# Optimization experiments

Hardware: AMD Instinct MI355X
Metric: run time of the kernel (lower is better)

The kernel has to match this reference:

```python
import jax, jax.numpy as jnp
import numpy as np

N = 50000
IN_CH = 64
HID_CH = 32
NEG_SLOPE = 0.2  # PyG GATConv default for attention LeakyReLU


def _glorot(key, shape):
    fan = shape[0] + shape[-1] if len(shape) > 1 else shape[0]
    s = jnp.sqrt(6.0 / fan)
    return jax.random.uniform(key, shape, jnp.float32, -s, s)


def setup_inputs() -> dict:
    key = jax.random.key(0)
    ks = jax.random.split(key, 20)
    x = jax.random.normal(ks[0], (N, IN_CH), jnp.float32)
    edge_index = jax.random.randint(ks[1], (2, 800000), 0, N, jnp.int64)
    dims = [(IN_CH, IN_CH), (IN_CH, HID_CH), (HID_CH, IN_CH), (IN_CH, IN_CH)]
    inp = {"x": x, "edge_index": edge_index}
    for i, (di, do) in enumerate(dims, 1):
        inp[f"w{i}"] = _glorot(ks[4 * i - 2], (di, do))
        inp[f"as{i}"] = _glorot(ks[4 * i - 1], (do,))
        inp[f"ad{i}"] = _glorot(ks[4 * i], (do,))
        inp[f"b{i}"] = jnp.zeros((do,), jnp.float32)
    return inp


def _gat_layer(x, src, dst, W, a_src, a_dst, b):
    # x: [N, di] -> h: [N, do]
    h = x @ W
    # per-edge attention logits (source + destination contributions)
    e = jax.nn.leaky_relu(h[src] @ a_src + h[dst] @ a_dst, NEG_SLOPE)  # [E]
    # numerically stable segment softmax over incoming edges per dst node
    m = jax.ops.segment_max(e, dst, num_segments=N)
    ex = jnp.exp(e - m[dst])
    denom = jax.ops.segment_sum(ex, dst, num_segments=N)
    alpha = ex / (denom[dst] + 1e-16)  # [E]
    out = jax.ops.segment_sum(alpha[:, None] * h[src], dst, num_segments=N)
    return out + b


def reference(x, edge_index, w1, as1, ad1, b1, w2, as2, ad2, b2,
              w3, as3, ad3, b3, w4, as4, ad4, b4):
    # PyG GATConv adds self-loops by default
    ar = jnp.arange(N, dtype=edge_index.dtype)
    src = jnp.concatenate([edge_index[0], ar])
    dst = jnp.concatenate([edge_index[1], ar])

    h1 = jax.nn.relu(_gat_layer(x, src, dst, w1, as1, ad1, b1))
    h = _gat_layer(h1, src, dst, w2, as2, ad2, b2)
    h3 = jax.nn.relu(h)
    h4 = jax.nn.relu(_gat_layer(h3, src, dst, w3, as3, ad3, b3))
    out = _gat_layer(h4, src, dst, w4, as4, ad4, b4)
    return (out, h)
```

## Files before the change

### kernel.cpp

```cpp
#include <hip/hip_runtime.h>
#include <hip/hip_fp16.h>
#include <math.h>

#define N_NODES 50000
#define N_EDGES 800000
#define E_TOT   850000
#define NEG_SLOPE 0.2f
#define NB_SCAN 49

typedef unsigned short u16;
typedef float f32x4 __attribute__((ext_vector_type(4)));

__global__ void csr_init(int* deg) {
    int i = blockIdx.x * blockDim.x + threadIdx.x;
    if (i < N_NODES) deg[i] = 0;
}

__global__ void csr_degree(const int* __restrict__ dst, int* __restrict__ deg,
                           u16* __restrict__ rank) {
    int e = blockIdx.x * blockDim.x + threadIdx.x;
    if (e >= E_TOT) return;
    int d = (e < N_EDGES) ? dst[e] : (e - N_EDGES);
    rank[e] = (u16)atomicAdd(&deg[d], 1);
}

__global__ void scan_p1(const int* __restrict__ deg, int* __restrict__ bsum) {
    __shared__ int red[1024];
    int i = blockIdx.x * 1024 + threadIdx.x;
    red[threadIdx.x] = (i < N_NODES) ? deg[i] : 0;
    __syncthreads();
    for (int off = 512; off >= 1; off >>= 1) {
        if (threadIdx.x < off) red[threadIdx.x] += red[threadIdx.x + off];
        __syncthreads();
    }
    if (threadIdx.x == 0) bsum[blockIdx.x] = red[0];
}

__global__ void scan_p3(const int* __restrict__ deg, const int* __restrict__ bsum,
                        int* __restrict__ offs) {
    __shared__ int s[1024];
    __shared__ int bofs;
    int i = blockIdx.x * 1024 + threadIdx.x;
    int v = (i < N_NODES) ? deg[i] : 0;
    s[threadIdx.x] = v;
    if (threadIdx.x < 64) {
        int d = (threadIdx.x < NB_SCAN) ? bsum[threadIdx.x] : 0;
        int p = d;
        for (int off = 1; off < 64; off <<= 1) {
            int u = __shfl_up(p, off, 64);
            if ((int)threadIdx.x >= off) p += u;
        }
        if ((int)threadIdx.x == (int)blockIdx.x) bofs = p - d;
        if (blockIdx.x == NB_SCAN - 1 && threadIdx.x == NB_SCAN - 1)
            offs[N_NODES] = p;
    }
    __syncthreads();
    for (int off = 1; off < 1024; off <<= 1) {
        int u = (threadIdx.x >= off) ? s[threadIdx.x - off] : 0;
        __syncthreads();
        s[threadIdx.x] += u;
        __syncthreads();
    }
    if (i < N_NODES) offs[i] = bofs + s[threadIdx.x] - v;
}

__global__ void csr_fill(const int* __restrict__ src, const int* __restrict__ dst,
                         const u16* __restrict__ rank, const int* __restrict__ offs,
                         u16* __restrict__ csr_src) {
    int e = blockIdx.x * blockDim.x + threadIdx.x;
    if (e >= E_TOT) return;
    int s, d;
    if (e < N_EDGES) { s = src[e]; d = dst[e]; } else { s = e - N_EDGES; d = s; }
    csr_src[offs[d] + rank[e]] = (u16)s;
}

template<int DI, int DO>
__global__ void gemm_proj(const float* __restrict__ X, const float* __restrict__ W,
                          const float* __restrict__ a_src, const float* __restrict__ a_dst,
                          __half* __restrict__ Hh, float* __restrict__ ssrc,
                          float* __restrict__ sdst) {
    const int TPN = DO / 4;
    const int NPB = 256 / TPN;
    __shared__ float sW[DI * DO];
    __shared__ float sX[NPB][DI + 1];
    const int tid = threadIdx.x;
    for (int i = tid; i < DI * DO / 4; i += 256)
        ((float4*)sW)[i] = ((const float4*)W)[i];
    const int base = blockIdx.x * NPB;
    for (int i = tid; i < NPB * DI; i += 256) {
        int r = i / DI, col = i % DI;
        int node = base + r;
        sX[r][col] = (node < N_NODES) ? X[(long)node * DI + col] : 0.0f;
    }
    __syncthreads();
    const int cq = tid % TPN;
    const int g  = tid / TPN;
    const int node = base + g;
    if (node >= N_NODES) return;
    float ax = 0.0f, ay = 0.0f, az = 0.0f, aw = 0.0f;
    const float4* sW4 = (const float4*)sW;
#pragma unroll
    for (int k = 0; k < DI; k++) {
        float xv = sX[g][k];
        float4 w4 = sW4[k * TPN + cq];
        ax = fmaf(xv, w4.x, ax); ay = fmaf(xv, w4.y, ay);
        az = fmaf(xv, w4.z, az); aw = fmaf(xv, w4.w, aw);
    }
    union { uint2 u; __half2 h2[2]; } pk;
    pk.h2[0] = __float22half2_rn(make_float2(ax, ay));
    pk.h2[1] = __float22half2_rn(make_float2(az, aw));
    ((uint2*)(Hh + (long)node * DO))[cq] = pk.u;

    float4 as4 = ((const float4*)a_src)[cq];
    float4 ad4 = ((const float4*)a_dst)[cq];
    float ps = ax * as4.x + ay * as4.y + az * as4.z + aw * as4.w;
    float pd = ax * ad4.x + ay * ad4.y + az * ad4.z + aw * ad4.w;
#pragma unroll
    for (int m = TPN / 2; m >= 1; m >>= 1) {
        ps += __shfl_xor(ps, m, TPN);
        pd += __shfl_xor(pd, m, TPN);
    }
    if (cq == 0) { ssrc[node] = ps; sdst[node] = pd; }
}

template<int DIN, int DOUT>
__global__ void gather_gemm(const __half* __restrict__ Hh_in,
                            const float* __restrict__ ssrc_in,
                            const float* __restrict__ sdst_in,
                            const int* __restrict__ offs,
                            const u16* __restrict__ csr_src,
                            const float* __restrict__ bias_in,
                            int relu_o, float* __restrict__ extra_out,
                            const float* __restrict__ W2,
                            const float* __restrict__ a_src2,
                            const float* __restrict__ a_dst2,
                            __half* __restrict__ Hh_out,
                            float* __restrict__ ssrc2, float* __restrict__ sdst2) {
    constexpr int G = DIN / 4;
    constexpr int L = DIN / 8;
    constexpr int NPB = 256 / G;
    constexpr int NC = 32 / G;
    constexpr int JS = G / 2;
    constexpr int LDSW = (DOUT > 0) ? DIN * DOUT : 1;
    __shared__ float sW[LDSW];
    if constexpr (DOUT > 0) {
        for (int i = threadIdx.x; i < DIN * DOUT / 4; i += 256)
            ((float4*)sW)[i] = ((const float4*)W2)[i];
        __syncthreads();
    }
    const int t = threadIdx.x;
    const int node = blockIdx.x * NPB + t / G;
    const int r = t % G;
    const int hr = r / L;
    const int q  = r % L;
    const bool valid = (node < N_NODES);
    const int beg = valid ? offs[node] : 0;
    const int end = valid ? offs[node + 1] : 0;
    const int deg = end - beg;
    const float sdv = valid ? sdst_in[node] : 0.0f;
    const uint4* H4 = (const uint4*)Hh_in;

    int   sc[NC];
    float exc[NC];
#pragma unroll
    for (int k = 0; k < NC; k++) { sc[k] = 0; exc[k] = 0.0f; }
#pragma unroll
    for (int k = 0; k < NC; k++) {
        if (k * G + r < deg) sc[k] = csr_src[beg + k * G + r];
    }
#pragma unroll
    for (int k = 0; k < NC; k++) {
        if (k * G + r < deg) {
            float v = ssrc_in[sc[k]] + sdv;
            v = (v > 0.0f) ? v : NEG_SLOPE * v;
            exc[k] = __expf(v);
        }
    }
    float den = 0.0f;
#pragma unroll
    for (int k = 0; k < NC; k++) den += exc[k];

    float acc8[8];
#pragma unroll
    for (int c = 0; c < 8; c++) acc8[c] = 0.0f;

    uint4 buf[NC * JS];
#pragma unroll
    for (int k = 0; k < NC; k++) {
#pragma unroll
        for (int j = 0; j < JS; j++) {
            int sa = __shfl(sc[k], 2 * j + hr, G);
            buf[k * JS + j] = H4[(long)sa * L + q];
        }
    }
#pragma unroll
    for (int k = 0; k < NC; k++) {
#pragma unroll
        for (int j = 0; j < JS; j++) {
            float ea = __shfl(exc[k], 2 * j + hr, G);
            union { uint4 u; __half2 h2[4]; } ua;
            ua.u = buf[k * JS + j];
            float2 f0 = __half22float2(ua.h2[0]), f1 = __half22float2(ua.h2[1]);
            float2 f2 = __half22float2(ua.h2[2]), f3 = __half22float2(ua.h2[3]);
            acc8[0] = fmaf(ea, f0.x, acc8[0]); acc8[1] = fmaf(ea, f0.y, acc8[1]);
            acc8[2] = fmaf(ea, f1.x, acc8[2]); acc8[3] = fmaf(ea, f1.y, acc8[3]);
            acc8[4] = fmaf(ea, f2.x, acc8[4]); acc8[5] = fmaf(ea, f2.y, acc8[5]);
            acc8[6] = fmaf(ea, f3.x, acc8[6]); acc8[7] = fmaf(ea, f3.y, acc8[7]);
        }
    }
    for (int cb = beg + NC * G; cb < end; cb += G) {
        int cnt = min(G, end - cb);
        int s2 = 0; float ex2 = 0.0f;
        if (r < cnt) {
            s2 = csr_src[cb + r];
            float v = ssrc_in[s2] + sdv;
            v = (v > 0.0f) ? v : NEG_SLOPE * v;
            ex2 = __expf(v);
        }
        den += ex2;
#pragma unroll
        for (int j = 0; j < JS; j++) {
            int   sa = __shfl(s2, 2 * j + hr, G);
            float ea = __shfl(ex2, 2 * j + hr, G);
            union { uint4 u; __half2 h2[4]; } ua;
            ua.u = H4[(long)sa * L + q];
            float2 f0 = __half22float2(ua.h2[0]), f1 = __half22float2(ua.h2[1]);
            float2 f2 = __half22float2(ua.h2[2]), f3 = __half22float2(ua.h2[3]);
            acc8[0] = fmaf(ea, f0.x, acc8[0]); acc8[1] = fmaf(ea, f0.y, acc8[1]);
            acc8[2] = fmaf(ea, f1.x, acc8[2]); acc8[3] = fmaf(ea, f1.y, acc8[3]);
            acc8[4] = fmaf(ea, f2.x, acc8[4]); acc8[5] = fmaf(ea, f2.y, acc8[5]);
            acc8[6] = fmaf(ea, f3.x, acc8[6]); acc8[7] = fmaf(ea, f3.y, acc8[7]);
        }
    }
#pragma unroll
    for (int c = 0; c < 8; c++) acc8[c] += __shfl_xor(acc8[c], L, G);
#pragma unroll
    for (int m = G / 2; m >= 1; m >>= 1) den += __shfl_xor(den, m, G);

    float inv = 1.0f / (den + 1e-16f);
    const float4* b4p = (const float4*)bias_in;
    float4 bq0 = b4p[2 * q], bq1 = b4p[2 * q + 1];
    float o8[8];
    o8[0] = acc8[0] * inv + bq0.x; o8[1] = acc8[1] * inv + bq0.y;
    o8[2] = acc8[2] * inv + bq0.z; o8[3] = acc8[3] * inv + bq0.w;
    o8[4] = acc8[4] * inv + bq1.x; o8[5] = acc8[5] * inv + bq1.y;
    o8[6] = acc8[6] * inv + bq1.z; o8[7] = acc8[7] * inv + bq1.w;
    if (valid && extra_out) {
        f32x4 st;
        if (hr == 0) { st.x = o8[0]; st.y = o8[1]; st.z = o8[2]; st.w = o8[3]; }
        else         { st.x = o8[4]; st.y = o8[5]; st.z = o8[6]; st.w = o8[7]; }
        __builtin_nontemporal_store(st,
            &((f32x4*)extra_out)[(long)node * (2 * L) + 2 * q + hr]);
    }
    if (relu_o) {
#pragma unroll
        for (int c = 0; c < 8; c++) o8[c] = fmaxf(o8[c], 0.0f);
    }

    if constexpr (DOUT > 0) {
        constexpr int C = DOUT / G;
        float acc2[C];
#pragma unroll
        for (int c = 0; c < C; c++) acc2[c] = 0.0f;
        const int cbase = r * C;
#pragma unroll
        for (int kb = 0; kb < L; kb++) {
            float v[8];
#pragma unroll
            for (int c8 = 0; c8 < 8; c8++) v[c8] = __shfl(o8[c8], kb, G);
#pragma unroll
            for (int c8 = 0; c8 < 8; c8++) {
                const float* wr = &sW[(8 * kb + c8) * DOUT + cbase];
#pragma unroll
                for (int c = 0; c < C; c++) acc2[c] = fmaf(v[c8], wr[c], acc2[c]);
            }
        }
        float ps = 0.0f, pd = 0.0f;
#pragma unroll
        for (int c = 0; c < C; c++) {
            ps = fmaf(acc2[c], a_src2[cbase + c], ps);
            pd = fmaf(acc2[c], a_dst2[cbase + c], pd);
        }
#pragma unroll
        for (int m = G / 2; m >= 1; m >>= 1) {
            ps += __shfl_xor(ps, m, G);
            pd += __shfl_xor(pd, m, G);
        }
        if (valid) {
            union { unsigned int u1; uint2 u2; uint4 u4; __half2 h[C / 2]; } pk;
#pragma unroll
            for (int c = 0; c < C; c += 2)
                pk.h[c / 2] = __float22half2_rn(make_float2(acc2[c], acc2[c + 1]));
            char* dp = (char*)(Hh_out + (long)node * DOUT + cbase);
            if constexpr (C == 2) *(unsigned int*)dp = pk.u1;
            else if constexpr (C == 4) *(uint2*)dp = pk.u2;
            else                        *(uint4*)dp = pk.u4;
            if (r == 0) { ssrc2[node] = ps; sdst2[node] = pd; }
        }
    }
}

extern "C" void kernel_launch(void* const* d_in, const int* in_sizes, int n_in,
                              void* d_out, int out_size, void* d_ws, size_t ws_size,
                              hipStream_t stream) {
    const float* x  = (const float*)d_in[0];
    const int*   ei = (const int*)d_in[1];

    const float* w1  = (const float*)d_in[2];
    const float* as1 = (const float*)d_in[3];
    const float* ad1 = (const float*)d_in[4];
    const float* b1  = (const float*)d_in[5];
    const float* w2  = (const float*)d_in[6];
    const float* as2 = (const float*)d_in[7];
    const float* ad2 = (const float*)d_in[8];
    const float* b2  = (const float*)d_in[9];
    const float* w3  = (const float*)d_in[10];
    const float* as3 = (const float*)d_in[11];
    const float* ad3 = (const float*)d_in[12];
    const float* b3  = (const float*)d_in[13];
    const float* w4  = (const float*)d_in[14];
    const float* as4 = (const float*)d_in[15];
    const float* ad4 = (const float*)d_in[16];
    const float* b4  = (const float*)d_in[17];

    float* out_final = (float*)d_out;
    float* out_h     = (float*)d_out + N_NODES * 64;

    float* ws    = (float*)d_ws;
    __half* Hh_a = (__half*)ws;
    __half* Hh_b = (__half*)(ws + N_NODES * 32);
    float* SS_a  = ws + 2 * N_NODES * 32;
    float* SD_a  = SS_a + N_NODES;
    float* SS_b  = SD_a + N_NODES;
    float* SD_b  = SS_b + N_NODES;
    int* deg     = (int*)(SD_b + N_NODES);
    u16* rank    = (u16*)(deg + N_NODES);
    int* offs    = (int*)(rank + E_TOT);
    u16* csr_src = (u16*)(offs + N_NODES + 1);
    int* bsum    = (int*)(csr_src + E_TOT);

    const int* src = ei;
    const int* dst = ei + N_EDGES;

    csr_init<<<(N_NODES + 255) / 256, 256, 0, stream>>>(deg);
    csr_degree<<<(E_TOT + 255) / 256, 256, 0, stream>>>(dst, deg, rank);
    scan_p1<<<NB_SCAN, 1024, 0, stream>>>(deg, bsum);
    scan_p3<<<NB_SCAN, 1024, 0, stream>>>(deg, bsum, offs);
    csr_fill<<<(E_TOT + 255) / 256, 256, 0, stream>>>(src, dst, rank, offs, csr_src);

    gemm_proj<64, 64><<<(N_NODES + 15) / 16, 256, 0, stream>>>(
        x, w1, as1, ad1, Hh_a, SS_a, SD_a);

    gather_gemm<64, 32><<<(N_NODES * 16 + 255) / 256, 256, 0, stream>>>(
        Hh_a, SS_a, SD_a, offs, csr_src, b1, 1, nullptr,
        w2, as2, ad2, Hh_b, SS_b, SD_b);
    gather_gemm<32, 64><<<(N_NODES * 8 + 255) / 256, 256, 0, stream>>>(
        Hh_b, SS_b, SD_b, offs, csr_src, b2, 1, out_h,
        w3, as3, ad3, Hh_a, SS_a, SD_a);
    gather_gemm<64, 64><<<(N_NODES * 16 + 255) / 256, 256, 0, stream>>>(
        Hh_a, SS_a, SD_a, offs, csr_src, b3, 1, nullptr,
        w4, as4, ad4, Hh_b, SS_b, SD_b);
    gather_gemm<64, 0><<<(N_NODES * 16 + 255) / 256, 256, 0, stream>>>(
        Hh_b, SS_b, SD_b, offs, csr_src, b4, 0, out_final,
        nullptr, nullptr, nullptr, nullptr, nullptr, nullptr);
}
```

Before: 262.4 us.

## Split 64-wide gathers into two source-half passes for cache locality

Partitions each node's CSR neighbor list into sources below and above the midpoint node index, and runs each 64-channel aggregation layer as two passes, one per source half. The first pass writes partial accumulators and denominators to a workspace buffer, and the second pass adds them back before finishing. The aim is to keep the gathered fp16 feature table for each pass small enough to stay resident in cache. The cost is an extra kernel launch per layer plus a full write and read of a 50000x64 float partial buffer.

```diff
diff --git a/kernel.cpp b/kernel.cpp
--- a/kernel.cpp
+++ b/kernel.cpp
@@ -7,27 +7,31 @@
 #define E_TOT   850000
 #define NEG_SLOPE 0.2f
 #define NB_SCAN 49
+#define HALF    25000
 
 typedef unsigned short u16;
 typedef float f32x4 __attribute__((ext_vector_type(4)));
 
-__global__ void csr_init(int* deg) {
+__global__ void csr_init(int* degAB) {
     int i = blockIdx.x * blockDim.x + threadIdx.x;
-    if (i < N_NODES) deg[i] = 0;
-}
-
-__global__ void csr_degree(const int* __restrict__ dst, int* __restrict__ deg,
+    if (i < 2 * N_NODES) degAB[i] = 0;
+}
+
+__global__ void csr_degree(const int* __restrict__ src, const int* __restrict__ dst,
+                           int* __restrict__ degA, int* __restrict__ degB,
                            u16* __restrict__ rank) {
     int e = blockIdx.x * blockDim.x + threadIdx.x;
     if (e >= E_TOT) return;
-    int d = (e < N_EDGES) ? dst[e] : (e - N_EDGES);
-    rank[e] = (u16)atomicAdd(&deg[d], 1);
-}
-
-__global__ void scan_p1(const int* __restrict__ deg, int* __restrict__ bsum) {
+    int s, d;
+    if (e < N_EDGES) { s = src[e]; d = dst[e]; } else { s = e - N_EDGES; d = s; }
+    rank[e] = (u16)atomicAdd((s < HALF) ? &degA[d] : &degB[d], 1);
+}
+
+__global__ void scan_p1(const int* __restrict__ degA, const int* __restrict__ degB,
+                        int* __restrict__ bsum) {
     __shared__ int red[1024];
     int i = blockIdx.x * 1024 + threadIdx.x;
-    red[threadIdx.x] = (i < N_NODES) ? deg[i] : 0;
+    red[threadIdx.x] = (i < N_NODES) ? degA[i] + degB[i] : 0;
     __syncthreads();
     for (int off = 512; off >= 1; off >>= 1) {
         if (threadIdx.x < off) red[threadIdx.x] += red[threadIdx.x + off];
@@ -36,12 +40,12 @@
     if (threadIdx.x == 0) bsum[blockIdx.x] = red[0];
 }
 
-__global__ void scan_p3(const int* __restrict__ deg, const int* __restrict__ bsum,
-                        int* __restrict__ offs) {
+__global__ void scan_p3(const int* __restrict__ degA, const int* __restrict__ degB,
+                        const int* __restrict__ bsum, int* __restrict__ offs) {
     __shared__ int s[1024];
     __shared__ int bofs;
     int i = blockIdx.x * 1024 + threadIdx.x;
-    int v = (i < N_NODES) ? deg[i] : 0;
+    int v = (i < N_NODES) ? degA[i] + degB[i] : 0;
     s[threadIdx.x] = v;
     if (threadIdx.x < 64) {
         int d = (threadIdx.x < NB_SCAN) ? bsum[threadIdx.x] : 0;
@@ -66,12 +70,13 @@
 
 __global__ void csr_fill(const int* __restrict__ src, const int* __restrict__ dst,
                          const u16* __restrict__ rank, const int* __restrict__ offs,
-                         u16* __restrict__ csr_src) {
+                         const int* __restrict__ degA, u16* __restrict__ csr_src) {
     int e = blockIdx.x * blockDim.x + threadIdx.x;
     if (e >= E_TOT) return;
     int s, d;
     if (e < N_EDGES) { s = src[e]; d = dst[e]; } else { s = e - N_EDGES; d = s; }
-    csr_src[offs[d] + rank[e]] = (u16)s;
+    int pos = offs[d] + ((s < HALF) ? (int)rank[e] : degA[d] + (int)rank[e]);
+    csr_src[pos] = (u16)s;
 }
 
 template<int DI, int DO>
@@ -123,12 +128,14 @@
     if (cq == 0) { ssrc[node] = ps; sdst[node] = pd; }
 }
 
-template<int DIN, int DOUT>
+template<int DIN, int PASS, int DOUT>
 __global__ void gather_gemm(const __half* __restrict__ Hh_in,
                             const float* __restrict__ ssrc_in,
                             const float* __restrict__ sdst_in,
                             const int* __restrict__ offs,
+                            const int* __restrict__ degA,
                             const u16* __restrict__ csr_src,
+                            float* __restrict__ accP, float* __restrict__ denP,
                             const float* __restrict__ bias_in,
                             int relu_o, float* __restrict__ extra_out,
                             const float* __restrict__ W2,
@@ -154,8 +161,11 @@
     const int hr = r / L;
     const int q  = r % L;
     const bool valid = (node < N_NODES);
-    const int beg = valid ? offs[node] : 0;
-    const int end = valid ? offs[node + 1] : 0;
+    const int beg0 = valid ? offs[node] : 0;
+    const int end0 = valid ? offs[node + 1] : 0;
+    int beg = beg0, end = end0;
+    if constexpr (PASS == 1) end = beg0 + (valid ? degA[node] : 0);
+    if constexpr (PASS == 2) beg = beg0 + (valid ? degA[node] : 0);
     const int deg = end - beg;
     const float sdv = valid ? sdst_in[node] : 0.0f;
     const uint4* H4 = (const uint4*)Hh_in;
@@ -165,9 +175,8 @@
 #pragma unroll
     for (int k = 0; k < NC; k++) { sc[k] = 0; exc[k] = 0.0f; }
 #pragma unroll
-    for (int k = 0; k < NC; k++) {
+    for (int k = 0; k < NC; k++)
         if (k * G + r < deg) sc[k] = csr_src[beg + k * G + r];
-    }
 #pragma unroll
     for (int k = 0; k < NC; k++) {
         if (k * G + r < deg) {
@@ -232,10 +241,34 @@
             acc8[6] = fmaf(ea, f3.x, acc8[6]); acc8[7] = fmaf(ea, f3.y, acc8[7]);
         }
     }
+
+    if constexpr (PASS == 2) {
+        if (valid && hr == 0) {
+            const f32x4* ap = (const f32x4*)(accP + (long)node * DIN + q * 8);
+            f32x4 p0 = __builtin_nontemporal_load(ap);
+            f32x4 p1 = __builtin_nontemporal_load(ap + 1);
+            acc8[0] += p0.x; acc8[1] += p0.y; acc8[2] += p0.z; acc8[3] += p0.w;
+            acc8[4] += p1.x; acc8[5] += p1.y; acc8[6] += p1.z; acc8[7] += p1.w;
+        }
+        if (valid && r == 0) den += __builtin_nontemporal_load(denP + node);
+    }
 #pragma unroll
     for (int c = 0; c < 8; c++) acc8[c] += __shfl_xor(acc8[c], L, G);
 #pragma unroll
     for (int m = G / 2; m >= 1; m >>= 1) den += __shfl_xor(den, m, G);
+
+    if constexpr (PASS == 1) {
+        if (valid && hr == 0) {
+            f32x4 s0v, s1v;
+            s0v.x = acc8[0]; s0v.y = acc8[1]; s0v.z = acc8[2]; s0v.w = acc8[3];
+            s1v.x = acc8[4]; s1v.y = acc8[5]; s1v.z = acc8[6]; s1v.w = acc8[7];
+            f32x4* ap = (f32x4*)(accP + (long)node * DIN + q * 8);
+            __builtin_nontemporal_store(s0v, ap);
+            __builtin_nontemporal_store(s1v, ap + 1);
+        }
+        if (valid && r == 0) __builtin_nontemporal_store(den, denP + node);
+        return;
+    }
 
     float inv = 1.0f / (den + 1e-16f);
     const float4* b4p = (const float4*)bias_in;
@@ -333,8 +366,11 @@
     float* SD_a  = SS_a + N_NODES;
     float* SS_b  = SD_a + N_NODES;
     float* SD_b  = SS_b + N_NODES;
-    int* deg     = (int*)(SD_b + N_NODES);
-    u16* rank    = (u16*)(deg + N_NODES);
+    float* accP  = SD_b + N_NODES;
+    float* denP  = accP + N_NODES * 64;
+    int* degA    = (int*)(denP + N_NODES);
+    int* degB    = degA + N_NODES;
+    u16* rank    = (u16*)(degB + N_NODES);
     int* offs    = (int*)(rank + E_TOT);
     u16* csr_src = (u16*)(offs + N_NODES + 1);
     int* bsum    = (int*)(csr_src + E_TOT);
@@ -342,25 +378,40 @@
     const int* src = ei;
     const int* dst = ei + N_EDGES;
 
-    csr_init<<<(N_NODES + 255) / 256, 256, 0, stream>>>(deg);
-    csr_degree<<<(E_TOT + 255) / 256, 256, 0, stream>>>(dst, deg, rank);
-    scan_p1<<<NB_SCAN, 1024, 0, stream>>>(deg, bsum);
-    scan_p3<<<NB_SCAN, 1024, 0, stream>>>(deg, bsum, offs);
-    csr_fill<<<(E_TOT + 255) / 256, 256, 0, stream>>>(src, dst, rank, offs, csr_src);
+    csr_init<<<(2 * N_NODES + 255) / 256, 256, 0, stream>>>(degA);
+    csr_degree<<<(E_TOT + 255) / 256, 256, 0, stream>>>(src, dst, degA, degB, rank);
+    scan_p1<<<NB_SCAN, 1024, 0, stream>>>(degA, degB, bsum);
+    scan_p3<<<NB_SCAN, 1024, 0, stream>>>(degA, degB, bsum, offs);
+    csr_fill<<<(E_TOT + 255) / 256, 256, 0, stream>>>(src, dst, rank, offs, degA, csr_src);
 
     gemm_proj<64, 64><<<(N_NODES + 15) / 16, 256, 0, stream>>>(
         x, w1, as1, ad1, Hh_a, SS_a, SD_a);
 
-    gather_gemm<64, 32><<<(N_NODES * 16 + 255) / 256, 256, 0, stream>>>(
-        Hh_a, SS_a, SD_a, offs, csr_src, b1, 1, nullptr,
-        w2, as2, ad2, Hh_b, SS_b, SD_b);
-    gather_gemm<32, 64><<<(N_NODES * 8 + 255) / 256, 256, 0, stream>>>(
-        Hh_b, SS_b, SD_b, offs, csr_src, b2, 1, out_h,
-        w3, as3, ad3, Hh_a, SS_a, SD_a);
-    gather_gemm<64, 64><<<(N_NODES * 16 + 255) / 256, 256, 0, stream>>>(
-        Hh_a, SS_a, SD_a, offs, csr_src, b3, 1, nullptr,
-        w4, as4, ad4, Hh_b, SS_b, SD_b);
-    gather_gemm<64, 0><<<(N_NODES * 16 + 255) / 256, 256, 0, stream>>>(
-        Hh_b, SS_b, SD_b, offs, csr_src, b4, 0, out_final,
-        nullptr, nullptr, nullptr, nullptr, nullptr, nullptr);
-}
+    const int gridA = (N_NODES * 16 + 255) / 256;
+    const int gridB = (N_NODES * 8 + 255) / 256;
+
+    gather_gemm<64, 1, 0><<<gridA, 256, 0, stream>>>(
+        Hh_a, SS_a, SD_a, offs, degA, csr_src, accP, denP,
+        nullptr, 0, nullptr, nullptr, nullptr, nullptr, nullptr, nullptr, nullptr);
+    gather_gemm<64, 2, 32><<<gridA, 256, 0, stream>>>(
+        Hh_a, SS_a, SD_a, offs, degA, csr_src, accP, denP,
+        b1, 1, nullptr, w2, as2, ad2, Hh_b, SS_b, SD_b);
+
+    gather_gemm<32, 0, 64><<<gridB, 256, 0, stream>>>(
+        Hh_b, SS_b, SD_b, offs, degA, csr_src, accP, denP,
+        b2, 1, out_h, w3, as3, ad3, Hh_a, SS_a, SD_a);
+
+    gather_gemm<64, 1, 0><<<gridA, 256, 0, stream>>>(
+        Hh_a, SS_a, SD_a, offs, degA, csr_src, accP, denP,
+        nullptr, 0, nullptr, nullptr, nullptr, nullptr, nullptr, nullptr, nullptr);
+    gather_gemm<64, 2, 64><<<gridA, 256, 0, stream>>>(
+        Hh_a, SS_a, SD_a, offs, degA, csr_src, accP, denP,
+        b3, 1, nullptr, w4, as4, ad4, Hh_b, SS_b, SD_b);
+
+    gather_gemm<64, 1, 0><<<gridA, 256, 0, stream>>>(
+        Hh_b, SS_b, SD_b, offs, degA, csr_src, accP, denP,
+        nullptr, 0, nullptr, nullptr, nullptr, nullptr, nullptr, nullptr, nullptr);
+    gather_gemm<64, 2, 0><<<gridA, 256, 0, stream>>>(
+        Hh_b, SS_b, SD_b, offs, degA, csr_src, accP, denP,
+        b4, 0, out_final, nullptr, nullptr, nullptr, nullptr, nullptr, nullptr);
+}
```

Result: slower. 309.9 us (+18.1%).

## Merge CSR build launches: lookback scan, fused fill+projection, memset init

Applied to the files above, without the earlier changes.

Cuts the launch count in the CSR construction phase. The two-pass scan becomes a single-pass decoupled-lookback scan that spins on packed flag/aggregate words. The CSR fill and first-layer projection GEMM now run as one kernel with disjoint block ranges, and the degree init kernel is replaced by hipMemsetAsync. The lookback scan relies on all 49 blocks being co-resident, and the spin loop adds a serial dependency between blocks.

```diff
diff --git a/kernel.cpp b/kernel.cpp
--- a/kernel.cpp
+++ b/kernel.cpp
@@ -7,14 +7,11 @@
 #define E_TOT   850000
 #define NEG_SLOPE 0.2f
 #define NB_SCAN 49
+#define FILL_NB ((E_TOT + 255) / 256)
+#define GEMM_NB ((N_NODES + 15) / 16)
 
 typedef unsigned short u16;
 typedef float f32x4 __attribute__((ext_vector_type(4)));
-
-__global__ void csr_init(int* deg) {
-    int i = blockIdx.x * blockDim.x + threadIdx.x;
-    if (i < N_NODES) deg[i] = 0;
-}
 
 __global__ void csr_degree(const int* __restrict__ dst, int* __restrict__ deg,
                            u16* __restrict__ rank) {
@@ -24,69 +21,63 @@
     rank[e] = (u16)atomicAdd(&deg[d], 1);
 }
 
-__global__ void scan_p1(const int* __restrict__ deg, int* __restrict__ bsum) {
-    __shared__ int red[1024];
-    int i = blockIdx.x * 1024 + threadIdx.x;
-    red[threadIdx.x] = (i < N_NODES) ? deg[i] : 0;
-    __syncthreads();
-    for (int off = 512; off >= 1; off >>= 1) {
-        if (threadIdx.x < off) red[threadIdx.x] += red[threadIdx.x + off];
-        __syncthreads();
-    }
-    if (threadIdx.x == 0) bsum[blockIdx.x] = red[0];
-}
-
-__global__ void scan_p3(const int* __restrict__ deg, const int* __restrict__ bsum,
-                        int* __restrict__ offs) {
+__global__ void scan_lookback(const int* __restrict__ deg,
+                              unsigned long long* __restrict__ aggPack,
+                              int* __restrict__ offs) {
     __shared__ int s[1024];
     __shared__ int bofs;
-    int i = blockIdx.x * 1024 + threadIdx.x;
+    const int bid = blockIdx.x, tid = threadIdx.x;
+    const int i = bid * 1024 + tid;
     int v = (i < N_NODES) ? deg[i] : 0;
-    s[threadIdx.x] = v;
-    if (threadIdx.x < 64) {
-        int d = (threadIdx.x < NB_SCAN) ? bsum[threadIdx.x] : 0;
-        int p = d;
-        for (int off = 1; off < 64; off <<= 1) {
-            int u = __shfl_up(p, off, 64);
-            if ((int)threadIdx.x >= off) p += u;
-        }
-        if ((int)threadIdx.x == (int)blockIdx.x) bofs = p - d;
-        if (blockIdx.x == NB_SCAN - 1 && threadIdx.x == NB_SCAN - 1)
-            offs[N_NODES] = p;
-    }
+    s[tid] = v;
     __syncthreads();
     for (int off = 1; off < 1024; off <<= 1) {
-        int u = (threadIdx.x >= off) ? s[threadIdx.x - off] : 0;
+        int u = (tid >= off) ? s[tid - off] : 0;
         __syncthreads();
-        s[threadIdx.x] += u;
+        s[tid] += u;
         __syncthreads();
     }
-    if (i < N_NODES) offs[i] = bofs + s[threadIdx.x] - v;
-}
-
-__global__ void csr_fill(const int* __restrict__ src, const int* __restrict__ dst,
-                         const u16* __restrict__ rank, const int* __restrict__ offs,
-                         u16* __restrict__ csr_src) {
-    int e = blockIdx.x * blockDim.x + threadIdx.x;
-    if (e >= E_TOT) return;
-    int s, d;
-    if (e < N_EDGES) { s = src[e]; d = dst[e]; } else { s = e - N_EDGES; d = s; }
-    csr_src[offs[d] + rank[e]] = (u16)s;
-}
-
-template<int DI, int DO>
-__global__ void gemm_proj(const float* __restrict__ X, const float* __restrict__ W,
+    const int agg = s[1023];
+    if (tid == 0) {
+        atomicExch(&aggPack[bid], (1ULL << 32) | (unsigned)agg);
+        long long running = 0;
+        for (int j = bid - 1; j >= 0; ) {
+            unsigned long long p;
+            do { p = atomicAdd(&aggPack[j], 0ULL); } while ((p >> 32) == 0);
+            running += (unsigned)(p & 0xffffffffu);
+            if ((p >> 32) == 2ULL) break;
+            j--;
+        }
+        atomicExch(&aggPack[bid], (2ULL << 32) | (unsigned)(running + agg));
+        bofs = (int)running;
+        if (bid == NB_SCAN - 1) offs[N_NODES] = (int)(running + agg);
+    }
+    __syncthreads();
+    if (i < N_NODES) offs[i] = bofs + s[tid] - v;
+}
+
+__global__ void fill_gemm(const int* __restrict__ src, const int* __restrict__ dst,
+                          const u16* __restrict__ rank, const int* __restrict__ offs,
+                          u16* __restrict__ csr_src,
+                          const float* __restrict__ X, const float* __restrict__ W,
                           const float* __restrict__ a_src, const float* __restrict__ a_dst,
                           __half* __restrict__ Hh, float* __restrict__ ssrc,
                           float* __restrict__ sdst) {
-    const int TPN = DO / 4;
-    const int NPB = 256 / TPN;
+    constexpr int DI = 64, DO = 64, TPN = DO / 4, NPB = 256 / TPN;
+    if (blockIdx.x < FILL_NB) {
+        int e = blockIdx.x * 256 + threadIdx.x;
+        if (e >= E_TOT) return;
+        int s, d;
+        if (e < N_EDGES) { s = src[e]; d = dst[e]; } else { s = e - N_EDGES; d = s; }
+        csr_src[offs[d] + rank[e]] = (u16)s;
+        return;
+    }
     __shared__ float sW[DI * DO];
     __shared__ float sX[NPB][DI + 1];
     const int tid = threadIdx.x;
     for (int i = tid; i < DI * DO / 4; i += 256)
         ((float4*)sW)[i] = ((const float4*)W)[i];
-    const int base = blockIdx.x * NPB;
+    const int base = (blockIdx.x - FILL_NB) * NPB;
     for (int i = tid; i < NPB * DI; i += 256) {
         int r = i / DI, col = i % DI;
         int node = base + r;
@@ -334,22 +325,20 @@
     float* SS_b  = SD_a + N_NODES;
     float* SD_b  = SS_b + N_NODES;
     int* deg     = (int*)(SD_b + N_NODES);
-    u16* rank    = (u16*)(deg + N_NODES);
+    unsigned long long* aggPack = (unsigned long long*)(deg + N_NODES);
+    u16* rank    = (u16*)(aggPack + 64);
     int* offs    = (int*)(rank + E_TOT);
     u16* csr_src = (u16*)(offs + N_NODES + 1);
-    int* bsum    = (int*)(csr_src + E_TOT);
 
     const int* src = ei;
     const int* dst = ei + N_EDGES;
 
-    csr_init<<<(N_NODES + 255) / 256, 256, 0, stream>>>(deg);
+    hipMemsetAsync(deg, 0, N_NODES * sizeof(int) + 64 * sizeof(unsigned long long),
+                   stream);
     csr_degree<<<(E_TOT + 255) / 256, 256, 0, stream>>>(dst, deg, rank);
-    scan_p1<<<NB_SCAN, 1024, 0, stream>>>(deg, bsum);
-    scan_p3<<<NB_SCAN, 1024, 0, stream>>>(deg, bsum, offs);
-    csr_fill<<<(E_TOT + 255) / 256, 256, 0, stream>>>(src, dst, rank, offs, csr_src);
-
-    gemm_proj<64, 64><<<(N_NODES + 15) / 16, 256, 0, stream>>>(
-        x, w1, as1, ad1, Hh_a, SS_a, SD_a);
+    scan_lookback<<<NB_SCAN, 1024, 0, stream>>>(deg, aggPack, offs);
+    fill_gemm<<<FILL_NB + GEMM_NB, 256, 0, stream>>>(
+        src, dst, rank, offs, csr_src, x, w1, as1, ad1, Hh_a, SS_a, SD_a);
 
     gather_gemm<64, 32><<<(N_NODES * 16 + 255) / 256, 256, 0, stream>>>(
         Hh_a, SS_a, SD_a, offs, csr_src, b1, 1, nullptr,
```

After: 258.3 us, median of 2. About the same (-1.6%).
